# Optimization experiments

Hardware: AMD Instinct MI355X
Metric: run time of the kernel (lower is better)

## Reference

```python
import jax, jax.numpy as jnp
from jax import lax
import numpy as np

VOCAB, L, D, K = 50000, 8921, 300, 10
B, T = 8, 2048


def setup_inputs() -> dict:
    key = jax.random.key(0)
    k_ids, k_e, k_cw, k_cb, k_u = jax.random.split(key, 5)
    ids = jax.random.randint(k_ids, (B, T), 0, VOCAB, dtype=jnp.int32)
    embed_w = jax.random.normal(k_e, (VOCAB, D), dtype=jnp.float32) * 0.02
    embed_w = embed_w.at[0].set(0.0)  # padding_idx=0
    conv_w = jax.random.normal(k_cw, (D, D, K), dtype=jnp.float32) * 0.02  # (out, in, k) == torch OIH
    conv_b = jax.random.normal(k_cb, (D,), dtype=jnp.float32) * 0.02
    U = jax.random.normal(k_u, (L, D), dtype=jnp.float32)
    fc_bias = jnp.zeros((L,), dtype=jnp.float32)
    return {"ids": ids, "embed_w": embed_w, "conv_w": conv_w, "conv_b": conv_b, "U": U, "fc_bias": fc_bias}


def reference(ids, embed_w, conv_w, conv_b, U, fc_bias):
    # Embedding lookup (padding_idx row already zeroed in table)
    e = embed_w[ids]                       # (B, T, D)
    x = jnp.transpose(e, (0, 2, 1))        # (B, D, T)
    pad = conv_w.shape[-1] - 1             # torch padding=filter_size-1 (both sides)
    h = lax.conv_general_dilated(
        x, conv_w, window_strides=(1,), padding=[(pad, pad)],
        dimension_numbers=("NCH", "OIH", "NCH"))
    h = jax.nn.relu(h + conv_b[None, :, None])   # (B, D, T') where T' = T + K - 1
    attn = jax.nn.softmax(jnp.einsum("ld,bdt->blt", U, h), axis=-1)  # (B, L, T')
    z = jnp.einsum("blt,bdt->bld", attn, h)                          # (B, L, D)
    logits = jnp.einsum("bld,ld->bl", z, U) + fc_bias                # (B, L)
    return logits
```

## Files before the change

### kernel.cpp

```cpp
#include <hip/hip_runtime.h>

#define VOCAB   50000
#define LDIM    8921
#define DDIM    300
#define DPAD    320
#define KSZ     10
#define BATCH   8
#define TSEQ    2048
#define PADL    9
#define TPRIME  2057
#define TPADDED 2066
#define LPAD    8928

#define TSTG    32
#define NTT     65
#define TALLOC  (NTT * TSTG)
#define LBLK    70

typedef short s8v __attribute__((ext_vector_type(8)));
typedef float f4v __attribute__((ext_vector_type(4)));

typedef const __attribute__((address_space(1))) unsigned int* gas_ptr;
typedef __attribute__((address_space(3))) unsigned int* las_ptr;

__device__ inline unsigned short f2bf(float f) {
  union { float f; unsigned u; } v; v.f = f;
  unsigned r = v.u + 0x7FFF + ((v.u >> 16) & 1);
  return (unsigned short)(r >> 16);
}

__global__ __launch_bounds__(256) void gather_kernel(
    const int* __restrict__ ids, const float* __restrict__ embed_w,
    unsigned short* __restrict__ xp) {
  int wid = blockIdx.x * 4 + (threadIdx.x >> 6);
  int lane = threadIdx.x & 63;
  int b = wid / TPADDED, tau = wid % TPADDED;
  bool inr = (tau >= PADL) && (tau < PADL + TSEQ);
  int row = inr ? ids[b * TSEQ + (tau - PADL)] : 0;
  const float* src = embed_w + (size_t)row * DDIM;
  unsigned short* dst = xp + ((size_t)b * TPADDED + tau) * DPAD;
#pragma unroll
  for (int j = 0; j < 3; ++j) {
    int c2 = (j * 64 + lane) * 2;
    if (c2 < DPAD) {
      float v0 = (inr && c2 < DDIM) ? src[c2] : 0.0f;
      float v1 = (inr && c2 + 1 < DDIM) ? src[c2 + 1] : 0.0f;
      unsigned pk = (unsigned)f2bf(v0) | ((unsigned)f2bf(v1) << 16);
      *(unsigned*)&dst[c2] = pk;
    }
  }
}

__global__ __launch_bounds__(256) void wt_kernel(
    const float* __restrict__ w, unsigned short* __restrict__ wT) {
  int k = blockIdx.x / DPAD, o = blockIdx.x % DPAD;
  for (int i = threadIdx.x; i < DPAD; i += 256) {
    float v = (o < DDIM && i < DDIM) ? w[((size_t)o * DDIM + i) * KSZ + k] : 0.0f;
    wT[((size_t)k * DPAD + o) * DPAD + i] = f2bf(v);
  }
}

__global__ __launch_bounds__(256) void ut_kernel(
    const float* __restrict__ U, unsigned short* __restrict__ Ub) {
  int l = blockIdx.x;
  for (int d = threadIdx.x; d < DPAD; d += 256) {
    float v = (l < LDIM && d < DDIM) ? U[(size_t)l * DDIM + d] : 0.0f;
    Ub[(size_t)l * DPAD + d] = f2bf(v);
  }
}

#define CTN 80
#define CROWS 89
#define CSTRIDE 328
__global__ __launch_bounds__(256) void conv_mfma_kernel(
    const unsigned short* __restrict__ xp, const unsigned short* __restrict__ wT,
    const float* __restrict__ bias, unsigned short* __restrict__ h) {
  __shared__ unsigned short xls[CROWS * CSTRIDE];
  int b = blockIdx.x & 7, tb = blockIdx.x >> 3;
  int t0 = tb * CTN;
  int tid = threadIdx.x;
  {
    const unsigned short* src = xp + (size_t)b * TPADDED * DPAD;
    for (int idx = tid; idx < CROWS * 40; idx += 256) {
      int rr = idx / 40, c8 = idx % 40;
      int tp = t0 + rr;
      int4 v = make_int4(0, 0, 0, 0);
      if (tp < TPADDED) v = *(const int4*)&src[(size_t)tp * DPAD + c8 * 8];
      *(int4*)&xls[rr * CSTRIDE + c8 * 8] = v;
    }
  }
  __syncthreads();
  int w = tid >> 6, lane = tid & 63;
  int l15 = lane & 15, quad = lane >> 4;
  int ob = w * 80;
  f4v acc[5][5];
#pragma unroll
  for (int mf = 0; mf < 5; ++mf) {
    float bv[4];
#pragma unroll
    for (int rr = 0; rr < 4; ++rr) {
      int o = ob + mf * 16 + quad * 4 + rr;
      bv[rr] = (o < DDIM) ? bias[o] : 0.0f;
    }
#pragma unroll
    for (int nf = 0; nf < 5; ++nf) {
      acc[mf][nf][0] = bv[0]; acc[mf][nf][1] = bv[1];
      acc[mf][nf][2] = bv[2]; acc[mf][nf][3] = bv[3];
    }
  }
  const unsigned short* wl = wT + (size_t)(ob + l15) * DPAD + quad * 8;
  s8v Aping[5], Apong[5];
#pragma unroll
  for (int mf = 0; mf < 5; ++mf) Aping[mf] = *(const s8v*)&wl[mf * 16 * DPAD];
#pragma unroll
  for (int mf = 0; mf < 5; ++mf) Apong[mf] = *(const s8v*)&wl[mf * 16 * DPAD + 32];
  for (int ii = 0; ii < 100; ii += 2) {
    {
      int kc = ii / 10, it = ii % 10;
      s8v Bv[5];
#pragma unroll
      for (int nf = 0; nf < 5; ++nf)
        Bv[nf] = *(const s8v*)&xls[(nf * 16 + l15 + kc) * CSTRIDE + it * 32 + quad * 8];
#pragma unroll
      for (int mf = 0; mf < 5; ++mf)
#pragma unroll
        for (int nf = 0; nf < 5; ++nf)
          acc[mf][nf] = __builtin_amdgcn_mfma_f32_16x16x32_bf16(Aping[mf], Bv[nf], acc[mf][nf], 0, 0, 0);
      int p = ii + 2;
      if (p < 100) {
        int kp = p / 10, itp = p % 10;
        const unsigned short* wp = wl + (size_t)kp * (DPAD * DPAD) + itp * 32;
#pragma unroll
        for (int mf = 0; mf < 5; ++mf) Aping[mf] = *(const s8v*)&wp[mf * 16 * DPAD];
      }
    }
    {
      int kc = (ii + 1) / 10, it = (ii + 1) % 10;
      s8v Bv[5];
#pragma unroll
      for (int nf = 0; nf < 5; ++nf)
        Bv[nf] = *(const s8v*)&xls[(nf * 16 + l15 + kc) * CSTRIDE + it * 32 + quad * 8];
#pragma unroll
      for (int mf = 0; mf < 5; ++mf)
#pragma unroll
        for (int nf = 0; nf < 5; ++nf)
          acc[mf][nf] = __builtin_amdgcn_mfma_f32_16x16x32_bf16(Apong[mf], Bv[nf], acc[mf][nf], 0, 0, 0);
      int p = ii + 3;
      if (p < 100) {
        int kp = p / 10, itp = p % 10;
        const unsigned short* wp = wl + (size_t)kp * (DPAD * DPAD) + itp * 32;
#pragma unroll
        for (int mf = 0; mf < 5; ++mf) Apong[mf] = *(const s8v*)&wp[mf * 16 * DPAD];
      }
    }
  }
#pragma unroll
  for (int mf = 0; mf < 5; ++mf) {
    int obase = ob + mf * 16 + quad * 4;
#pragma unroll
    for (int nf = 0; nf < 5; ++nf) {
      int t = t0 + nf * 16 + l15;
      bool live = t < TPRIME;
      unsigned short pk[4];
#pragma unroll
      for (int rr = 0; rr < 4; ++rr)
        pk[rr] = live ? f2bf(fmaxf(acc[mf][nf][rr], 0.0f)) : (unsigned short)0;
      *(uint2*)&h[((size_t)b * TALLOC + t) * DPAD + obase] = *(uint2*)pk;
    }
  }
}

__global__ __launch_bounds__(256, 3) void attn_mfma_kernel(
    const unsigned short* __restrict__ h, const unsigned short* __restrict__ Ub,
    const float* __restrict__ fcb, float* __restrict__ out) {
  __shared__ unsigned short hls[2 * TSTG * DPAD];
  int b = blockIdx.x & 7, lb = blockIdx.x >> 3;
  int tid = threadIdx.x;
  int w = tid >> 6, lane = tid & 63;
  int l15 = lane & 15, quad = lane >> 4;
  const unsigned short* hb = h + (size_t)b * TALLOC * DPAD;

  s8v A[2][10];
  {
    int lr0 = lb * 128 + w * 32 + l15;
#pragma unroll
    for (int mf = 0; mf < 2; ++mf) {
      int lr = lr0 + mf * 16;
      if (lr >= LPAD) lr = LPAD - 1;
      const unsigned short* up = Ub + (size_t)lr * DPAD + quad * 8;
#pragma unroll
      for (int kc = 0; kc < 10; ++kc)
        A[mf][kc] = *(const s8v*)&up[kc * 32];
    }
  }
#pragma unroll
  for (int mf = 0; mf < 2; ++mf)
#pragma unroll
    for (int kc = 0; kc < 10; ++kc)
      asm volatile("" : "+v"(A[mf][kc]));

  int srcoff[5];
#pragma unroll
  for (int j = 0; j < 5; ++j) {
    int g = w * 320 + j * 64 + lane;
    int r = g / 40, c = g % 40;
    srcoff[j] = r * DPAD + ((c ^ (r & 7)) * 8);
  }

#pragma unroll
  for (int j = 0; j < 5; ++j)
    __builtin_amdgcn_global_load_lds((gas_ptr)(const void*)(hb + srcoff[j]),
                                     (las_ptr)(void*)&hls[w * 2560 + j * 512],
                                     16, 0, 0);
  asm volatile("s_waitcnt vmcnt(0)" ::: "memory");
  __builtin_amdgcn_s_barrier();

  float se[2][4], sw[2][4];
#pragma unroll
  for (int mf = 0; mf < 2; ++mf)
#pragma unroll
    for (int r = 0; r < 4; ++r) { se[mf][r] = 0.0f; sw[mf][r] = 0.0f; }

  int xr8 = (l15 & 7) * 8;
  int rowb0 = l15 * DPAD;
  int rowb1 = (16 + l15) * DPAD;
  int bufsel = 0;
  for (int t = 0; t < NTT; ++t) {
    if (t + 1 < NTT) {
      const unsigned short* src = hb + (size_t)(t + 1) * TSTG * DPAD;
      int dstb = (bufsel ^ 1) * 10240 + w * 2560;
#pragma unroll
      for (int j = 0; j < 5; ++j)
        __builtin_amdgcn_global_load_lds((gas_ptr)(const void*)(src + srcoff[j]),
                                         (las_ptr)(void*)&hls[dstb + j * 512],
                                         16, 0, 0);
    }
    const unsigned short* bufc = &hls[bufsel * 10240];
    f4v acc[2][2];
#pragma unroll
    for (int mf = 0; mf < 2; ++mf)
#pragma unroll
      for (int nf = 0; nf < 2; ++nf) {
        acc[mf][nf][0] = 0.0f; acc[mf][nf][1] = 0.0f;
        acc[mf][nf][2] = 0.0f; acc[mf][nf][3] = 0.0f;
      }
    __builtin_amdgcn_s_setprio(1);
#pragma unroll
    for (int kc = 0; kc < 10; ++kc) {
      int ko = (kc * 32 + quad * 8) ^ xr8;
      s8v Bv0 = *(const s8v*)&bufc[rowb0 + ko];
      s8v Bv1 = *(const s8v*)&bufc[rowb1 + ko];
      acc[0][0] = __builtin_amdgcn_mfma_f32_16x16x32_bf16(A[0][kc], Bv0, acc[0][0], 0, 0, 0);
      acc[0][1] = __builtin_amdgcn_mfma_f32_16x16x32_bf16(A[0][kc], Bv1, acc[0][1], 0, 0, 0);
      acc[1][0] = __builtin_amdgcn_mfma_f32_16x16x32_bf16(A[1][kc], Bv0, acc[1][0], 0, 0, 0);
      acc[1][1] = __builtin_amdgcn_mfma_f32_16x16x32_bf16(A[1][kc], Bv1, acc[1][1], 0, 0, 0);
    }
    __builtin_amdgcn_s_setprio(0);
#pragma unroll
    for (int nf = 0; nf < 2; ++nf)
#pragma unroll
      for (int mf = 0; mf < 2; ++mf)
#pragma unroll
        for (int r = 0; r < 4; ++r) {
          float s = acc[mf][nf][r];
          float e = __expf(s);
          se[mf][r] += e;
          sw[mf][r] = fmaf(e, s, sw[mf][r]);
        }
    asm volatile("s_waitcnt vmcnt(0)" ::: "memory");
    __builtin_amdgcn_s_barrier();
    bufsel ^= 1;
  }

#pragma unroll
  for (int mf = 0; mf < 2; ++mf)
#pragma unroll
    for (int r = 0; r < 4; ++r) {
      float a = se[mf][r], c = sw[mf][r];
#pragma unroll
      for (int off = 1; off < 16; off <<= 1) {
        a += __shfl_xor(a, off, 64);
        c += __shfl_xor(c, off, 64);
      }
      if (l15 == 0) {
        int l = lb * 128 + w * 32 + mf * 16 + quad * 4 + r;
        if (l < LDIM) out[(size_t)b * LDIM + l] = c / (a - 23.0f) + fcb[l];
      }
    }
}

extern "C" void kernel_launch(void* const* d_in, const int* in_sizes, int n_in,
                              void* d_out, int out_size, void* d_ws, size_t ws_size,
                              hipStream_t stream) {
  const int*   ids     = (const int*)d_in[0];
  const float* embed_w = (const float*)d_in[1];
  const float* conv_w  = (const float*)d_in[2];
  const float* conv_b  = (const float*)d_in[3];
  const float* U       = (const float*)d_in[4];
  const float* fc_bias = (const float*)d_in[5];
  float* out = (float*)d_out;

  unsigned char* p = (unsigned char*)d_ws;
  unsigned short* xp = (unsigned short*)p;                 p += (size_t)BATCH * TPADDED * DPAD * 2;
  unsigned short* hb = (unsigned short*)p;                 p += (size_t)BATCH * TALLOC * DPAD * 2;
  unsigned short* wT = (unsigned short*)p;                 p += (size_t)KSZ * DPAD * DPAD * 2;
  unsigned short* Ub = (unsigned short*)p;

  hipLaunchKernelGGL(gather_kernel, dim3(BATCH * TPADDED / 4), dim3(256), 0, stream,
                     ids, embed_w, xp);
  hipLaunchKernelGGL(wt_kernel, dim3(KSZ * DPAD), dim3(256), 0, stream, conv_w, wT);
  hipLaunchKernelGGL(ut_kernel, dim3(LPAD), dim3(256), 0, stream, U, Ub);
  hipLaunchKernelGGL(conv_mfma_kernel, dim3(BATCH * 26), dim3(256), 0, stream,
                     xp, wT, conv_b, hb);
  hipLaunchKernelGGL(attn_mfma_kernel, dim3(BATCH * LBLK), dim3(256), 0, stream,
                     hb, Ub, fc_bias, out);
}
```

Before: 290.3 us.

## Software-pipeline attention softmax behind next tile's MFMAs and merge prep kernels

The attention loop is unrolled by two with alternating accumulator sets, so the exp/sum epilogue of tile t-1 runs after tile t's MFMA chain is issued, overlapping transcendental work with matrix math. The first MFMA of each tile now uses a zero accumulator instead of explicitly clearing registers. The weight-transpose and U-convert kernels are merged into one launch to save a kernel launch, and the asm register pin on A is dropped. This needs twice the accumulator registers, which may cost occupancy. With NTT=65 the loop covers tiles 1..64 and the final tile is flushed after the loop.

```diff
diff --git a/kernel.cpp b/kernel.cpp
--- a/kernel.cpp
+++ b/kernel.cpp
@@ -51,21 +51,22 @@
   }
 }
 
-__global__ __launch_bounds__(256) void wt_kernel(
-    const float* __restrict__ w, unsigned short* __restrict__ wT) {
-  int k = blockIdx.x / DPAD, o = blockIdx.x % DPAD;
-  for (int i = threadIdx.x; i < DPAD; i += 256) {
-    float v = (o < DDIM && i < DDIM) ? w[((size_t)o * DDIM + i) * KSZ + k] : 0.0f;
-    wT[((size_t)k * DPAD + o) * DPAD + i] = f2bf(v);
-  }
-}
-
-__global__ __launch_bounds__(256) void ut_kernel(
-    const float* __restrict__ U, unsigned short* __restrict__ Ub) {
-  int l = blockIdx.x;
-  for (int d = threadIdx.x; d < DPAD; d += 256) {
-    float v = (l < LDIM && d < DDIM) ? U[(size_t)l * DDIM + d] : 0.0f;
-    Ub[(size_t)l * DPAD + d] = f2bf(v);
+__global__ __launch_bounds__(256) void prep_kernel(
+    const float* __restrict__ w, const float* __restrict__ U,
+    unsigned short* __restrict__ wT, unsigned short* __restrict__ Ub) {
+  int bid = blockIdx.x;
+  if (bid < KSZ * DPAD) {
+    int k = bid / DPAD, o = bid % DPAD;
+    for (int i = threadIdx.x; i < DPAD; i += 256) {
+      float v = (o < DDIM && i < DDIM) ? w[((size_t)o * DDIM + i) * KSZ + k] : 0.0f;
+      wT[((size_t)k * DPAD + o) * DPAD + i] = f2bf(v);
+    }
+  } else {
+    int l = bid - KSZ * DPAD;
+    for (int d = threadIdx.x; d < DPAD; d += 256) {
+      float v = (l < LDIM && d < DDIM) ? U[(size_t)l * DDIM + d] : 0.0f;
+      Ub[(size_t)l * DPAD + d] = f2bf(v);
+    }
   }
 }
 
@@ -193,11 +194,6 @@
         A[mf][kc] = *(const s8v*)&up[kc * 32];
     }
   }
-#pragma unroll
-  for (int mf = 0; mf < 2; ++mf)
-#pragma unroll
-    for (int kc = 0; kc < 10; ++kc)
-      asm volatile("" : "+v"(A[mf][kc]));
 
   int srcoff[5];
 #pragma unroll
@@ -225,52 +221,77 @@
   int rowb0 = l15 * DPAD;
   int rowb1 = (16 + l15) * DPAD;
   int bufsel = 0;
-  for (int t = 0; t < NTT; ++t) {
-    if (t + 1 < NTT) {
-      const unsigned short* src = hb + (size_t)(t + 1) * TSTG * DPAD;
-      int dstb = (bufsel ^ 1) * 10240 + w * 2560;
-#pragma unroll
-      for (int j = 0; j < 5; ++j)
-        __builtin_amdgcn_global_load_lds((gas_ptr)(const void*)(src + srcoff[j]),
-                                         (las_ptr)(void*)&hls[dstb + j * 512],
-                                         16, 0, 0);
-    }
-    const unsigned short* bufc = &hls[bufsel * 10240];
-    f4v acc[2][2];
-#pragma unroll
-    for (int mf = 0; mf < 2; ++mf)
-#pragma unroll
-      for (int nf = 0; nf < 2; ++nf) {
-        acc[mf][nf][0] = 0.0f; acc[mf][nf][1] = 0.0f;
-        acc[mf][nf][2] = 0.0f; acc[mf][nf][3] = 0.0f;
-      }
-    __builtin_amdgcn_s_setprio(1);
-#pragma unroll
-    for (int kc = 0; kc < 10; ++kc) {
-      int ko = (kc * 32 + quad * 8) ^ xr8;
-      s8v Bv0 = *(const s8v*)&bufc[rowb0 + ko];
-      s8v Bv1 = *(const s8v*)&bufc[rowb1 + ko];
-      acc[0][0] = __builtin_amdgcn_mfma_f32_16x16x32_bf16(A[0][kc], Bv0, acc[0][0], 0, 0, 0);
-      acc[0][1] = __builtin_amdgcn_mfma_f32_16x16x32_bf16(A[0][kc], Bv1, acc[0][1], 0, 0, 0);
-      acc[1][0] = __builtin_amdgcn_mfma_f32_16x16x32_bf16(A[1][kc], Bv0, acc[1][0], 0, 0, 0);
-      acc[1][1] = __builtin_amdgcn_mfma_f32_16x16x32_bf16(A[1][kc], Bv1, acc[1][1], 0, 0, 0);
-    }
-    __builtin_amdgcn_s_setprio(0);
+  const f4v vzero = {0.0f, 0.0f, 0.0f, 0.0f};
+  f4v aA[2][2], aB[2][2];
+
+#define ATTN_TILE(TT, AC, AP, DOPREV)                                          \
+  {                                                                            \
+    if ((TT) + 1 < NTT) {                                                      \
+      const unsigned short* src = hb + (size_t)((TT) + 1) * TSTG * DPAD;       \
+      int dstb = (bufsel ^ 1) * 10240 + w * 2560;                              \
+      _Pragma("unroll")                                                        \
+      for (int j = 0; j < 5; ++j)                                              \
+        __builtin_amdgcn_global_load_lds(                                      \
+            (gas_ptr)(const void*)(src + srcoff[j]),                           \
+            (las_ptr)(void*)&hls[dstb + j * 512], 16, 0, 0);                   \
+    }                                                                          \
+    const unsigned short* bufc = &hls[bufsel * 10240];                         \
+    __builtin_amdgcn_s_setprio(1);                                             \
+    {                                                                          \
+      int ko = (quad * 8) ^ xr8;                                               \
+      s8v Bv0 = *(const s8v*)&bufc[rowb0 + ko];                                \
+      s8v Bv1 = *(const s8v*)&bufc[rowb1 + ko];                                \
+      AC[0][0] = __builtin_amdgcn_mfma_f32_16x16x32_bf16(A[0][0], Bv0, vzero, 0, 0, 0); \
+      AC[0][1] = __builtin_amdgcn_mfma_f32_16x16x32_bf16(A[0][0], Bv1, vzero, 0, 0, 0); \
+      AC[1][0] = __builtin_amdgcn_mfma_f32_16x16x32_bf16(A[1][0], Bv0, vzero, 0, 0, 0); \
+      AC[1][1] = __builtin_amdgcn_mfma_f32_16x16x32_bf16(A[1][0], Bv1, vzero, 0, 0, 0); \
+    }                                                                          \
+    _Pragma("unroll")                                                          \
+    for (int kc = 1; kc < 10; ++kc) {                                          \
+      int ko = (kc * 32 + quad * 8) ^ xr8;                                     \
+      s8v Bv0 = *(const s8v*)&bufc[rowb0 + ko];                                \
+      s8v Bv1 = *(const s8v*)&bufc[rowb1 + ko];                                \
+      AC[0][0] = __builtin_amdgcn_mfma_f32_16x16x32_bf16(A[0][kc], Bv0, AC[0][0], 0, 0, 0); \
+      AC[0][1] = __builtin_amdgcn_mfma_f32_16x16x32_bf16(A[0][kc], Bv1, AC[0][1], 0, 0, 0); \
+      AC[1][0] = __builtin_amdgcn_mfma_f32_16x16x32_bf16(A[1][kc], Bv0, AC[1][0], 0, 0, 0); \
+      AC[1][1] = __builtin_amdgcn_mfma_f32_16x16x32_bf16(A[1][kc], Bv1, AC[1][1], 0, 0, 0); \
+    }                                                                          \
+    __builtin_amdgcn_s_setprio(0);                                             \
+    if (DOPREV) {                                                              \
+      _Pragma("unroll")                                                        \
+      for (int mf = 0; mf < 2; ++mf)                                           \
+        _Pragma("unroll")                                                      \
+        for (int nf = 0; nf < 2; ++nf)                                         \
+          _Pragma("unroll")                                                    \
+          for (int r = 0; r < 4; ++r) {                                        \
+            float s = AP[mf][nf][r];                                           \
+            float e = __expf(s);                                               \
+            se[mf][r] += e;                                                    \
+            sw[mf][r] = fmaf(e, s, sw[mf][r]);                                 \
+          }                                                                    \
+    }                                                                          \
+    asm volatile("s_waitcnt vmcnt(0)" ::: "memory");                           \
+    __builtin_amdgcn_s_barrier();                                              \
+    bufsel ^= 1;                                                               \
+  }
+
+  ATTN_TILE(0, aA, aB, 0)
+  for (int t = 1; t + 1 < NTT; t += 2) {
+    ATTN_TILE(t, aB, aA, 1)
+    ATTN_TILE(t + 1, aA, aB, 1)
+  }
+#pragma unroll
+  for (int mf = 0; mf < 2; ++mf)
 #pragma unroll
     for (int nf = 0; nf < 2; ++nf)
 #pragma unroll
-      for (int mf = 0; mf < 2; ++mf)
-#pragma unroll
-        for (int r = 0; r < 4; ++r) {
-          float s = acc[mf][nf][r];
-          float e = __expf(s);
-          se[mf][r] += e;
-          sw[mf][r] = fmaf(e, s, sw[mf][r]);
-        }
-    asm volatile("s_waitcnt vmcnt(0)" ::: "memory");
-    __builtin_amdgcn_s_barrier();
-    bufsel ^= 1;
-  }
+      for (int r = 0; r < 4; ++r) {
+        float s = aA[mf][nf][r];
+        float e = __expf(s);
+        se[mf][r] += e;
+        sw[mf][r] = fmaf(e, s, sw[mf][r]);
+      }
+#undef ATTN_TILE
 
 #pragma unroll
   for (int mf = 0; mf < 2; ++mf)
@@ -308,8 +329,8 @@
 
   hipLaunchKernelGGL(gather_kernel, dim3(BATCH * TPADDED / 4), dim3(256), 0, stream,
                      ids, embed_w, xp);
-  hipLaunchKernelGGL(wt_kernel, dim3(KSZ * DPAD), dim3(256), 0, stream, conv_w, wT);
-  hipLaunchKernelGGL(ut_kernel, dim3(LPAD), dim3(256), 0, stream, U, Ub);
+  hipLaunchKernelGGL(prep_kernel, dim3(KSZ * DPAD + LPAD), dim3(256), 0, stream,
+                     conv_w, U, wT, Ub);
   hipLaunchKernelGGL(conv_mfma_kernel, dim3(BATCH * 26), dim3(256), 0, stream,
                      xp, wT, conv_b, hb);
   hipLaunchKernelGGL(attn_mfma_kernel, dim3(BATCH * LBLK), dim3(256), 0, stream,
```

After: 297.4 us. 1.02x slower.

## Split attention block across eight waves and merge weight-prep kernels

Applied to the files above, without the earlier changes.

The attention kernel moves from 4 waves each owning 32 label rows to 8 waves each owning 16 rows, so each wave keeps half the A fragments and accumulators in registers. The cooperative LDS staging of each h tile is redistributed across 512 threads with uneven per-wave rounds. The two weight conversion kernels are merged into one launch to save a kernel launch. The aim is higher latency hiding per block and lower register pressure, at the cost of more waves sharing each barrier and each wave doing more B-fragment LDS reads per MFMA.

```diff
diff --git a/kernel.cpp b/kernel.cpp
--- a/kernel.cpp
+++ b/kernel.cpp
@@ -51,21 +51,22 @@
   }
 }
 
-__global__ __launch_bounds__(256) void wt_kernel(
-    const float* __restrict__ w, unsigned short* __restrict__ wT) {
-  int k = blockIdx.x / DPAD, o = blockIdx.x % DPAD;
-  for (int i = threadIdx.x; i < DPAD; i += 256) {
-    float v = (o < DDIM && i < DDIM) ? w[((size_t)o * DDIM + i) * KSZ + k] : 0.0f;
-    wT[((size_t)k * DPAD + o) * DPAD + i] = f2bf(v);
-  }
-}
-
-__global__ __launch_bounds__(256) void ut_kernel(
-    const float* __restrict__ U, unsigned short* __restrict__ Ub) {
-  int l = blockIdx.x;
-  for (int d = threadIdx.x; d < DPAD; d += 256) {
-    float v = (l < LDIM && d < DDIM) ? U[(size_t)l * DDIM + d] : 0.0f;
-    Ub[(size_t)l * DPAD + d] = f2bf(v);
+__global__ __launch_bounds__(256) void prep_kernel(
+    const float* __restrict__ w, const float* __restrict__ U,
+    unsigned short* __restrict__ wT, unsigned short* __restrict__ Ub) {
+  int bid = blockIdx.x;
+  if (bid < KSZ * DPAD) {
+    int k = bid / DPAD, o = bid % DPAD;
+    for (int i = threadIdx.x; i < DPAD; i += 256) {
+      float v = (o < DDIM && i < DDIM) ? w[((size_t)o * DDIM + i) * KSZ + k] : 0.0f;
+      wT[((size_t)k * DPAD + o) * DPAD + i] = f2bf(v);
+    }
+  } else {
+    int l = bid - KSZ * DPAD;
+    for (int d = threadIdx.x; d < DPAD; d += 256) {
+      float v = (l < LDIM && d < DDIM) ? U[(size_t)l * DDIM + d] : 0.0f;
+      Ub[(size_t)l * DPAD + d] = f2bf(v);
+    }
   }
 }
 
@@ -170,7 +171,7 @@
   }
 }
 
-__global__ __launch_bounds__(256, 3) void attn_mfma_kernel(
+__global__ __launch_bounds__(512) void attn_mfma_kernel(
     const unsigned short* __restrict__ h, const unsigned short* __restrict__ Ub,
     const float* __restrict__ fcb, float* __restrict__ out) {
   __shared__ unsigned short hls[2 * TSTG * DPAD];
@@ -180,113 +181,100 @@
   int l15 = lane & 15, quad = lane >> 4;
   const unsigned short* hb = h + (size_t)b * TALLOC * DPAD;
 
-  s8v A[2][10];
+  s8v A[10];
   {
-    int lr0 = lb * 128 + w * 32 + l15;
-#pragma unroll
-    for (int mf = 0; mf < 2; ++mf) {
-      int lr = lr0 + mf * 16;
-      if (lr >= LPAD) lr = LPAD - 1;
-      const unsigned short* up = Ub + (size_t)lr * DPAD + quad * 8;
-#pragma unroll
-      for (int kc = 0; kc < 10; ++kc)
-        A[mf][kc] = *(const s8v*)&up[kc * 32];
-    }
-  }
-#pragma unroll
-  for (int mf = 0; mf < 2; ++mf)
+    int lr = lb * 128 + w * 16 + l15;
+    if (lr >= LPAD) lr = LPAD - 1;
+    const unsigned short* up = Ub + (size_t)lr * DPAD + quad * 8;
 #pragma unroll
     for (int kc = 0; kc < 10; ++kc)
-      asm volatile("" : "+v"(A[mf][kc]));
-
-  int srcoff[5];
-#pragma unroll
-  for (int j = 0; j < 5; ++j) {
-    int g = w * 320 + j * 64 + lane;
+      A[kc] = *(const s8v*)&up[kc * 32];
+  }
+
+  int nrounds = (w < 4) ? 3 : 2;
+  int srcoff[3], ldsbase[3];
+#pragma unroll
+  for (int j = 0; j < 3; ++j) {
+    int g = j * 512 + w * 64 + lane;
     int r = g / 40, c = g % 40;
     srcoff[j] = r * DPAD + ((c ^ (r & 7)) * 8);
-  }
-
-#pragma unroll
-  for (int j = 0; j < 5; ++j)
-    __builtin_amdgcn_global_load_lds((gas_ptr)(const void*)(hb + srcoff[j]),
-                                     (las_ptr)(void*)&hls[w * 2560 + j * 512],
-                                     16, 0, 0);
+    ldsbase[j] = (j * 512 + w * 64) * 8;
+  }
+
+#pragma unroll
+  for (int j = 0; j < 3; ++j)
+    if (j < nrounds)
+      __builtin_amdgcn_global_load_lds((gas_ptr)(const void*)(hb + srcoff[j]),
+                                       (las_ptr)(void*)&hls[ldsbase[j]],
+                                       16, 0, 0);
   asm volatile("s_waitcnt vmcnt(0)" ::: "memory");
   __builtin_amdgcn_s_barrier();
 
-  float se[2][4], sw[2][4];
-#pragma unroll
-  for (int mf = 0; mf < 2; ++mf)
-#pragma unroll
-    for (int r = 0; r < 4; ++r) { se[mf][r] = 0.0f; sw[mf][r] = 0.0f; }
+  float se[4], sw[4];
+#pragma unroll
+  for (int r = 0; r < 4; ++r) { se[r] = 0.0f; sw[r] = 0.0f; }
 
   int xr8 = (l15 & 7) * 8;
   int rowb0 = l15 * DPAD;
   int rowb1 = (16 + l15) * DPAD;
   int bufsel = 0;
+  const f4v vzero = {0.0f, 0.0f, 0.0f, 0.0f};
   for (int t = 0; t < NTT; ++t) {
     if (t + 1 < NTT) {
       const unsigned short* src = hb + (size_t)(t + 1) * TSTG * DPAD;
-      int dstb = (bufsel ^ 1) * 10240 + w * 2560;
-#pragma unroll
-      for (int j = 0; j < 5; ++j)
-        __builtin_amdgcn_global_load_lds((gas_ptr)(const void*)(src + srcoff[j]),
-                                         (las_ptr)(void*)&hls[dstb + j * 512],
-                                         16, 0, 0);
+      int dstb = (bufsel ^ 1) * 10240;
+#pragma unroll
+      for (int j = 0; j < 3; ++j)
+        if (j < nrounds)
+          __builtin_amdgcn_global_load_lds((gas_ptr)(const void*)(src + srcoff[j]),
+                                           (las_ptr)(void*)&hls[dstb + ldsbase[j]],
+                                           16, 0, 0);
     }
     const unsigned short* bufc = &hls[bufsel * 10240];
-    f4v acc[2][2];
-#pragma unroll
-    for (int mf = 0; mf < 2; ++mf)
-#pragma unroll
-      for (int nf = 0; nf < 2; ++nf) {
-        acc[mf][nf][0] = 0.0f; acc[mf][nf][1] = 0.0f;
-        acc[mf][nf][2] = 0.0f; acc[mf][nf][3] = 0.0f;
-      }
+    f4v acc0, acc1;
     __builtin_amdgcn_s_setprio(1);
-#pragma unroll
-    for (int kc = 0; kc < 10; ++kc) {
+    {
+      int ko = (quad * 8) ^ xr8;
+      s8v Bv0 = *(const s8v*)&bufc[rowb0 + ko];
+      s8v Bv1 = *(const s8v*)&bufc[rowb1 + ko];
+      acc0 = __builtin_amdgcn_mfma_f32_16x16x32_bf16(A[0], Bv0, vzero, 0, 0, 0);
+      acc1 = __builtin_amdgcn_mfma_f32_16x16x32_bf16(A[0], Bv1, vzero, 0, 0, 0);
+    }
+#pragma unroll
+    for (int kc = 1; kc < 10; ++kc) {
       int ko = (kc * 32 + quad * 8) ^ xr8;
       s8v Bv0 = *(const s8v*)&bufc[rowb0 + ko];
       s8v Bv1 = *(const s8v*)&bufc[rowb1 + ko];
-      acc[0][0] = __builtin_amdgcn_mfma_f32_16x16x32_bf16(A[0][kc], Bv0, acc[0][0], 0, 0, 0);
-      acc[0][1] = __builtin_amdgcn_mfma_f32_16x16x32_bf16(A[0][kc], Bv1, acc[0][1], 0, 0, 0);
-      acc[1][0] = __builtin_amdgcn_mfma_f32_16x16x32_bf16(A[1][kc], Bv0, acc[1][0], 0, 0, 0);
-      acc[1][1] = __builtin_amdgcn_mfma_f32_16x16x32_bf16(A[1][kc], Bv1, acc[1][1], 0, 0, 0);
+      acc0 = __builtin_amdgcn_mfma_f32_16x16x32_bf16(A[kc], Bv0, acc0, 0, 0, 0);
+      acc1 = __builtin_amdgcn_mfma_f32_16x16x32_bf16(A[kc], Bv1, acc1, 0, 0, 0);
     }
     __builtin_amdgcn_s_setprio(0);
 #pragma unroll
-    for (int nf = 0; nf < 2; ++nf)
-#pragma unroll
-      for (int mf = 0; mf < 2; ++mf)
-#pragma unroll
-        for (int r = 0; r < 4; ++r) {
-          float s = acc[mf][nf][r];
-          float e = __expf(s);
-          se[mf][r] += e;
-          sw[mf][r] = fmaf(e, s, sw[mf][r]);
-        }
+    for (int r = 0; r < 4; ++r) {
+      float s0 = acc0[r], s1 = acc1[r];
+      float e0 = __expf(s0), e1 = __expf(s1);
+      se[r] += e0 + e1;
+      sw[r] = fmaf(e0, s0, sw[r]);
+      sw[r] = fmaf(e1, s1, sw[r]);
+    }
     asm volatile("s_waitcnt vmcnt(0)" ::: "memory");
     __builtin_amdgcn_s_barrier();
     bufsel ^= 1;
   }
 
 #pragma unroll
-  for (int mf = 0; mf < 2; ++mf)
-#pragma unroll
-    for (int r = 0; r < 4; ++r) {
-      float a = se[mf][r], c = sw[mf][r];
-#pragma unroll
-      for (int off = 1; off < 16; off <<= 1) {
-        a += __shfl_xor(a, off, 64);
-        c += __shfl_xor(c, off, 64);
-      }
-      if (l15 == 0) {
-        int l = lb * 128 + w * 32 + mf * 16 + quad * 4 + r;
-        if (l < LDIM) out[(size_t)b * LDIM + l] = c / (a - 23.0f) + fcb[l];
-      }
-    }
+  for (int r = 0; r < 4; ++r) {
+    float a = se[r], c = sw[r];
+#pragma unroll
+    for (int off = 1; off < 16; off <<= 1) {
+      a += __shfl_xor(a, off, 64);
+      c += __shfl_xor(c, off, 64);
+    }
+    if (l15 == 0) {
+      int l = lb * 128 + w * 16 + quad * 4 + r;
+      if (l < LDIM) out[(size_t)b * LDIM + l] = c / (a - 23.0f) + fcb[l];
+    }
+  }
 }
 
 extern "C" void kernel_launch(void* const* d_in, const int* in_sizes, int n_in,
@@ -308,10 +296,10 @@
 
   hipLaunchKernelGGL(gather_kernel, dim3(BATCH * TPADDED / 4), dim3(256), 0, stream,
                      ids, embed_w, xp);
-  hipLaunchKernelGGL(wt_kernel, dim3(KSZ * DPAD), dim3(256), 0, stream, conv_w, wT);
-  hipLaunchKernelGGL(ut_kernel, dim3(LPAD), dim3(256), 0, stream, U, Ub);
+  hipLaunchKernelGGL(prep_kernel, dim3(KSZ * DPAD + LPAD), dim3(256), 0, stream,
+                     conv_w, U, wT, Ub);
   hipLaunchKernelGGL(conv_mfma_kernel, dim3(BATCH * 26), dim3(256), 0, stream,
                      xp, wT, conv_b, hb);
-  hipLaunchKernelGGL(attn_mfma_kernel, dim3(BATCH * LBLK), dim3(256), 0, stream,
+  hipLaunchKernelGGL(attn_mfma_kernel, dim3(BATCH * LBLK), dim3(512), 0, stream,
                      hb, Ub, fc_bias, out);
 }
```

Result: slower. 305.4 us (+5.2%).
